# Kernel optimization log

Measured on AMD Instinct MI355X. Metric: run time of the kernel, lower is better.

Reference implementation:

```python
import jax, jax.numpy as jnp
import numpy as np

N = 100000   # nodes
E = 1600000  # edges (avg degree 16)
IN = 128     # in_feats
H = 4        # num_heads
D = 32       # out_feats per head
HD = H * D   # 128
LN_EPS = 1e-5


def setup_inputs() -> dict:
    key = jax.random.key(0)
    ks = jax.random.split(key, 16)
    w = lambda k, shp: (jax.random.normal(k, shp, dtype=jnp.float32) * 0.05)
    feat = jax.random.normal(ks[0], (N, IN), dtype=jnp.float32)
    src = jax.random.randint(ks[1], (E,), 0, N, dtype=jnp.int32)
    # ensure every destination node has >=1 incoming edge (no 0-in-degree)
    dst = jnp.concatenate([
        jnp.arange(N, dtype=jnp.int32),
        jax.random.randint(ks[2], (E - N,), 0, N, dtype=jnp.int32),
    ])
    return {
        "feat": feat, "src": src, "dst": dst,
        "Wq": w(ks[3], (IN, HD)), "bq": jnp.zeros((HD,), jnp.float32),
        "Wk": w(ks[4], (IN, HD)), "bk": jnp.zeros((HD,), jnp.float32),
        "Wv": w(ks[5], (IN, HD)), "bv": jnp.zeros((HD,), jnp.float32),
        "Wskip": w(ks[6], (IN, HD)), "bskip": jnp.zeros((HD,), jnp.float32),
        "Wgate": w(ks[7], (3 * HD, 1)), "bgate": jnp.zeros((1,), jnp.float32),
        "gamma": jnp.ones((HD,), jnp.float32), "beta": jnp.zeros((HD,), jnp.float32),
        "prelu_a": jnp.asarray(0.25, jnp.float32),
    }


def reference(feat, src, dst, Wq, bq, Wk, bk, Wv, bv, Wskip, bskip,
              Wgate, bgate, gamma, beta, prelu_a):
    n = feat.shape[0]
    q = (feat @ Wq + bq).reshape(n, H, D)   # src-side 'ft'
    k = (feat @ Wk + bk).reshape(n, H, D)   # dst-side 'ft'
    v = (feat @ Wv + bv).reshape(n, H, D)
    # edge scores: u_dot_v per head, scaled by 1/sqrt(D)
    a = jnp.einsum('ehd,ehd->eh', q[src], k[dst]) / jnp.sqrt(jnp.float32(D))  # [E,H]
    # edge_softmax: softmax over incoming edges of each destination node
    m = jax.ops.segment_max(a, dst, num_segments=n)          # [N,H]
    ex = jnp.exp(a - m[dst])                                  # [E,H]
    den = jax.ops.segment_sum(ex, dst, num_segments=n)        # [N,H]
    sa = ex / den[dst]                                        # [E,H]
    # weighted scatter-sum aggregation: sum_e sa * v[src] -> dst
    agg = jax.ops.segment_sum(sa[:, :, None] * v[src], dst, num_segments=n)
    rst = agg.reshape(n, HD)
    # skip connection + gate
    skip = feat @ Wskip + bskip
    g = jax.nn.sigmoid(jnp.concatenate([skip, rst, skip - rst], axis=-1) @ Wgate + bgate)
    rst = g * skip + (1.0 - g) * rst
    # layer norm
    mu = jnp.mean(rst, axis=-1, keepdims=True)
    var = jnp.mean(jnp.square(rst - mu), axis=-1, keepdims=True)
    rst = (rst - mu) * jax.lax.rsqrt(var + LN_EPS) * gamma + beta
    # PReLU (single shared slope)
    return jnp.where(rst > 0, rst, prelu_a * rst)
```

## Files before the change

### kernel.cpp

```cpp
#include <hip/hip_runtime.h>
#include <hip/hip_bf16.h>
#include <hip/hip_fp16.h>
#include <math.h>

#define N_NODES 100000
#define N_EDGES 1600000
#define NBUK 196
#define NSB  256
#define EPB  6250

typedef __attribute__((ext_vector_type(8))) short bf16x8;
typedef __attribute__((ext_vector_type(4))) float f32x4;
typedef __attribute__((ext_vector_type(2))) float f32x2;

__device__ __forceinline__ short f2bf_s(float x) {
    __hip_bfloat16 b = __float2bfloat16(x);
    return *reinterpret_cast<short*>(&b);
}
__device__ __forceinline__ __half2 bc2(unsigned u) {
    return *reinterpret_cast<__half2*>(&u);
}
__device__ __forceinline__ unsigned bcu(__half2 h) {
    return *reinterpret_cast<unsigned*>(&h);
}
__device__ __forceinline__ unsigned pack2h(float a, float b) {
    __half ha = __float2half(a), hb = __float2half(b);
    return (unsigned)*reinterpret_cast<unsigned short*>(&ha)
         | ((unsigned)*reinterpret_cast<unsigned short*>(&hb) << 16);
}

__global__ __launch_bounds__(256) void hist2_wt(
    const int* __restrict__ dst,
    const float* __restrict__ Wq, const float* __restrict__ Wk,
    const float* __restrict__ Wv, const float* __restrict__ Ws,
    int* __restrict__ histT, unsigned short* __restrict__ Wtb)
{
    int bid = blockIdx.x, tid = threadIdx.x;
    if (bid < NSB) {
        __shared__ int h[4 * NBUK];
        for (int t = tid; t < 4 * NBUK; t += 256) h[t] = 0;
        __syncthreads();
        int w = tid >> 6;
        for (int i = tid; i < EPB; i += 256)
            atomicAdd(&h[w * NBUK + (dst[bid * EPB + i] >> 9)], 1);
        __syncthreads();
        if (tid < NBUK)
            histT[tid * NSB + bid] = h[tid] + h[NBUK + tid]
                                   + h[2 * NBUK + tid] + h[3 * NBUK + tid];
    } else {
        int j = (bid - NSB) * 256 + tid;
        int m = j >> 14;
        int rem = j & 16383;
        int c = rem >> 7;
        int kk = rem & 127;
        const float* W = (m == 0) ? Wq : (m == 1) ? Wk : (m == 2) ? Wv : Ws;
        Wtb[j] = (unsigned short)f2bf_s(W[(size_t)kk * 128 + c]);
    }
}

__global__ __launch_bounds__(256) void scan_block2(
    const int* __restrict__ in, int* __restrict__ outlocal, int* __restrict__ bsums)
{
    __shared__ int s[256];
    int i = blockIdx.x * 256 + threadIdx.x;
    int x = in[i];
    s[threadIdx.x] = x;
    __syncthreads();
    #pragma unroll
    for (int o = 1; o < 256; o <<= 1) {
        int t = (threadIdx.x >= o) ? s[threadIdx.x - o] : 0;
        __syncthreads();
        s[threadIdx.x] += t;
        __syncthreads();
    }
    outlocal[i] = s[threadIdx.x] - x;
    if (threadIdx.x == 255) bsums[blockIdx.x] = s[255];
}

__global__ __launch_bounds__(512) void scan_sums2(
    const int* __restrict__ bsums, int* __restrict__ bscan)
{
    __shared__ int s[512];
    int i = threadIdx.x;
    int x = (i < NBUK) ? bsums[i] : 0;
    s[i] = x;
    __syncthreads();
    #pragma unroll
    for (int o = 1; o < 512; o <<= 1) {
        int t = (i >= o) ? s[i - o] : 0;
        __syncthreads();
        s[i] += t;
        __syncthreads();
    }
    if (i < NBUK) bscan[i] = s[i] - x;
}

__global__ __launch_bounds__(256) void scatter2(
    const int* __restrict__ src, const int* __restrict__ dst,
    const int* __restrict__ boffs, const int* __restrict__ bscan,
    unsigned* __restrict__ tmp)
{
    __shared__ int cur[NBUK];
    int bid = blockIdx.x, tid = threadIdx.x;
    if (tid < NBUK) cur[tid] = 0;
    __syncthreads();
    for (int i = tid; i < EPB; i += 256) {
        int e = bid * EPB + i;
        int d = dst[e];
        int s = src[e];
        int j = d >> 9;
        int r = atomicAdd(&cur[j], 1);
        int pos = boffs[j * NSB + bid] + bscan[j] + r;
        tmp[pos] = ((unsigned)(d & 511) << 17) | (unsigned)s;
    }
}

__global__ __launch_bounds__(256) void bucket_sort(
    const unsigned* __restrict__ tmp, const int* __restrict__ bscan,
    int* __restrict__ sorted_src, int* __restrict__ offs)
{
    int j = blockIdx.x, tid = threadIdx.x;
    int base = bscan[j];
    int next = (j == NBUK - 1) ? N_EDGES : bscan[j + 1];
    int cnt = next - base;

    __shared__ int h[512];
    __shared__ int o_[512];
    __shared__ int s_[256];

    h[tid] = 0; h[tid + 256] = 0;
    __syncthreads();
    for (int i = tid; i < cnt; i += 256)
        atomicAdd(&h[tmp[base + i] >> 17], 1);
    __syncthreads();

    int a0 = h[2 * tid], a1 = h[2 * tid + 1];
    s_[tid] = a0 + a1;
    __syncthreads();
    #pragma unroll
    for (int o = 1; o < 256; o <<= 1) {
        int t = (tid >= o) ? s_[tid - o] : 0;
        __syncthreads();
        s_[tid] += t;
        __syncthreads();
    }
    int eb = s_[tid] - a0 - a1;
    o_[2 * tid] = eb;
    o_[2 * tid + 1] = eb + a0;
    __syncthreads();

    for (int t = tid; t < 512; t += 256) {
        int n = j * 512 + t;
        if (n < N_NODES) offs[n] = base + o_[t];
    }
    __syncthreads();

    for (int i = tid; i < cnt; i += 256) {
        unsigned rec = tmp[base + i];
        int r = atomicAdd(&o_[rec >> 17], 1);
        sorted_src[base + r] = (int)((rec & 0x1FFFFu) << 7);
    }
}

__global__ __launch_bounds__(256) void gemm_mfma(
    const float* __restrict__ feat, const unsigned short* __restrict__ Wtb,
    const float* __restrict__ bq, const float* __restrict__ bk,
    const float* __restrict__ bv, const float* __restrict__ bs,
    unsigned char* __restrict__ q8, __half* __restrict__ vh,
    __half* __restrict__ ks_)
{
    __shared__ __align__(16) unsigned short Atile[32][136];
    __shared__ __align__(16) unsigned char  Oq8[32][144];
    __shared__ __align__(16) unsigned char  Ovh[32][272];
    __shared__ __align__(16) unsigned char  Oks[32][528];

    const int tid = threadIdx.x;
    const int r0  = blockIdx.x * 32;

    {
        int row = tid >> 3;
        int cg  = (tid & 7) * 16;
        const float4* fp = (const float4*)(feat + (size_t)(r0 + row) * 128 + cg);
        float4 f0 = fp[0], f1 = fp[1], f2 = fp[2], f3 = fp[3];
        unsigned short* ap = &Atile[row][cg];
        ap[0]  = (unsigned short)f2bf_s(f0.x); ap[1]  = (unsigned short)f2bf_s(f0.y);
        ap[2]  = (unsigned short)f2bf_s(f0.z); ap[3]  = (unsigned short)f2bf_s(f0.w);
        ap[4]  = (unsigned short)f2bf_s(f1.x); ap[5]  = (unsigned short)f2bf_s(f1.y);
        ap[6]  = (unsigned short)f2bf_s(f1.z); ap[7]  = (unsigned short)f2bf_s(f1.w);
        ap[8]  = (unsigned short)f2bf_s(f2.x); ap[9]  = (unsigned short)f2bf_s(f2.y);
        ap[10] = (unsigned short)f2bf_s(f2.z); ap[11] = (unsigned short)f2bf_s(f2.w);
        ap[12] = (unsigned short)f2bf_s(f3.x); ap[13] = (unsigned short)f2bf_s(f3.y);
        ap[14] = (unsigned short)f2bf_s(f3.z); ap[15] = (unsigned short)f2bf_s(f3.w);
    }
    __syncthreads();

    const int mat = tid >> 6;
    const int l   = tid & 63;
    const int lr  = l & 15;
    const int lg  = l >> 4;
    const float* bias = (mat == 0) ? bq : (mat == 1) ? bk : (mat == 2) ? bv : bs;

    f32x4 acc[2][8];
    #pragma unroll
    for (int i = 0; i < 2; i++)
        #pragma unroll
        for (int j = 0; j < 8; j++) acc[i][j] = (f32x4){0.f, 0.f, 0.f, 0.f};

    #pragma unroll
    for (int kks = 0; kks < 4; kks++) {
        const int k0 = kks * 32 + lg * 8;
        bf16x8 a[2], b[8];
        #pragma unroll
        for (int rf = 0; rf < 2; rf++)
            a[rf] = *(const bf16x8*)&Atile[rf * 16 + lr][k0];
        #pragma unroll
        for (int cf = 0; cf < 8; cf++) {
            int col = cf * 16 + lr;
            b[cf] = *(const bf16x8*)(Wtb + ((size_t)mat * 128 + col) * 128 + k0);
        }
        #pragma unroll
        for (int rf = 0; rf < 2; rf++)
            #pragma unroll
            for (int cf = 0; cf < 8; cf++)
                acc[rf][cf] = __builtin_amdgcn_mfma_f32_16x16x32_bf16(
                    b[cf], a[rf], acc[rf][cf], 0, 0, 0);
    }

    #pragma unroll
    for (int rf = 0; rf < 2; rf++) {
        int rl = rf * 16 + lr;
        #pragma unroll
        for (int cf = 0; cf < 8; cf++) {
            int colb = cf * 16 + lg * 4;
            float4 b4 = *(const float4*)(bias + colb);
            float a0 = acc[rf][cf][0] + b4.x, a1 = acc[rf][cf][1] + b4.y;
            float a2 = acc[rf][cf][2] + b4.z, a3 = acc[rf][cf][3] + b4.w;
            if (mat == 0) {
                unsigned u = (unsigned)__builtin_amdgcn_cvt_pk_fp8_f32(a0, a1, 0, false);
                u = (unsigned)__builtin_amdgcn_cvt_pk_fp8_f32(a2, a3, (int)u, true);
                *(unsigned*)&Oq8[rl][colb] = u;
            } else if (mat == 2) {
                uint2 pk; pk.x = pack2h(a0, a1); pk.y = pack2h(a2, a3);
                *(uint2*)&Ovh[rl][colb * 2] = pk;
            } else {
                uint2 pk; pk.x = pack2h(a0, a1); pk.y = pack2h(a2, a3);
                *(uint2*)&Oks[rl][((mat == 3) ? 256 : 0) + colb * 2] = pk;
            }
        }
    }
    __syncthreads();

    {
        int row = tid >> 3;
        int c16 = (tid & 7) * 16;
        *(uint4*)(q8 + (size_t)(r0 + row) * 128 + c16) = *(const uint4*)&Oq8[row][c16];
        {
            char* gp = (char*)vh + (size_t)(r0 + row) * 256 + (tid & 7) * 32;
            const char* lp = (const char*)&Ovh[row][0] + (tid & 7) * 32;
            ((uint4*)gp)[0] = ((const uint4*)lp)[0];
            ((uint4*)gp)[1] = ((const uint4*)lp)[1];
        }
        {
            char* gp = (char*)ks_ + (size_t)(r0 + row) * 512 + (tid & 7) * 64;
            const char* lp = (const char*)&Oks[row][0] + (tid & 7) * 64;
            ((uint4*)gp)[0] = ((const uint4*)lp)[0];
            ((uint4*)gp)[1] = ((const uint4*)lp)[1];
            ((uint4*)gp)[2] = ((const uint4*)lp)[2];
            ((uint4*)gp)[3] = ((const uint4*)lp)[3];
        }
    }
}

__global__ __launch_bounds__(256) void node_fused(
    const unsigned char* __restrict__ q8, const __half* __restrict__ vh,
    const __half* __restrict__ ks_,
    const int* __restrict__ offs, const int* __restrict__ sorted_src,
    const float* __restrict__ wg, const float* __restrict__ bg,
    const float* __restrict__ gamma, const float* __restrict__ beta,
    const float* __restrict__ pa, float* __restrict__ out)
{
    int wid = threadIdx.x >> 6;
    int l   = threadIdx.x & 63;
    int qtr = l >> 4;
    int c   = l & 15;
    int n = blockIdx.x * 4 + wid;
    if (n >= N_NODES) return;

    int start = offs[n];
    int end   = (n + 1 < N_NODES) ? offs[n + 1] : N_EDGES;

    const uint4* krow = (const uint4*)ks_;
    uint4 kp  = krow[(size_t)n * 32 + c];
    uint4 sp4 = krow[(size_t)n * 32 + 16 + c];

    float kf[8];
    {
        __half2 h;
        h = bc2(kp.x); kf[0] = __low2float(h); kf[1] = __high2float(h);
        h = bc2(kp.y); kf[2] = __low2float(h); kf[3] = __high2float(h);
        h = bc2(kp.z); kf[4] = __low2float(h); kf[5] = __high2float(h);
        h = bc2(kp.w); kf[6] = __low2float(h); kf[7] = __high2float(h);
    }

    float den = 0.f;
    __half2 ag0 = bc2(0u), ag1 = bc2(0u), ag2 = bc2(0u), ag3 = bc2(0u);
    const float C = 0.25503483f;

    const char* qb = (const char*)q8 + c * 8;
    const char* vb = (const char*)vh + c * 16;

    int base = start;
    int sA = sorted_src[min(base + qtr, end - 1)];
    uint2 qA = *(const uint2*)(qb + sA);
    uint4 vA = *(const uint4*)(vb + 2 * (size_t)sA);
    bool hasB = (base + 4) < end;
    uint2 qB; uint4 vB;
    if (hasB) {
        int sB = sorted_src[min(base + 4 + qtr, end - 1)];
        qB = *(const uint2*)(qb + sB);
        vB = *(const uint4*)(vb + 2 * (size_t)sB);
    }
    int sC = ((base + 8) < end) ? sorted_src[min(base + 8 + qtr, end - 1)] : 0;

    for (;;) {
        bool hasC = (base + 8) < end;
        uint2 qC; uint4 vC;
        if (hasC) {
            qC = *(const uint2*)(qb + sC);
            vC = *(const uint4*)(vb + 2 * (size_t)sC);
        }
        int sD = ((base + 12) < end) ? sorted_src[min(base + 12 + qtr, end - 1)] : 0;

        f32x2 q01 = __builtin_amdgcn_cvt_pk_f32_fp8((int)qA.x, false);
        f32x2 q23 = __builtin_amdgcn_cvt_pk_f32_fp8((int)qA.x, true);
        f32x2 q45 = __builtin_amdgcn_cvt_pk_f32_fp8((int)qA.y, false);
        f32x2 q67 = __builtin_amdgcn_cvt_pk_f32_fp8((int)qA.y, true);
        float d = q01.x * kf[0] + q01.y * kf[1] + q23.x * kf[2] + q23.y * kf[3]
                + q45.x * kf[4] + q45.y * kf[5] + q67.x * kf[6] + q67.y * kf[7];
        d += __shfl_xor(d, 1);
        d += __shfl_xor(d, 2);
        float e = (base + qtr < end) ? __builtin_amdgcn_exp2f(d * C) : 0.f;
        den += e;
        __half2 e2 = __float2half2_rn(e);
        ag0 = __hfma2(e2, bc2(vA.x), ag0);
        ag1 = __hfma2(e2, bc2(vA.y), ag1);
        ag2 = __hfma2(e2, bc2(vA.z), ag2);
        ag3 = __hfma2(e2, bc2(vA.w), ag3);

        if (!hasB) break;
        base += 4;
        qA = qB; vA = vB; qB = qC; vB = vC; sC = sD; hasB = hasC;
    }

    den += __shfl_xor(den, 16);
    den += __shfl_xor(den, 32);
    ag0 = __hadd2(ag0, bc2(__shfl_xor(bcu(ag0), 16)));
    ag1 = __hadd2(ag1, bc2(__shfl_xor(bcu(ag1), 16)));
    ag2 = __hadd2(ag2, bc2(__shfl_xor(bcu(ag2), 16)));
    ag3 = __hadd2(ag3, bc2(__shfl_xor(bcu(ag3), 16)));
    ag0 = __hadd2(ag0, bc2(__shfl_xor(bcu(ag0), 32)));
    ag1 = __hadd2(ag1, bc2(__shfl_xor(bcu(ag1), 32)));
    ag2 = __hadd2(ag2, bc2(__shfl_xor(bcu(ag2), 32)));
    ag3 = __hadd2(ag3, bc2(__shfl_xor(bcu(ag3), 32)));

    float rd = 1.f / den;
    float r[8];
    r[0] = __low2float(ag0) * rd; r[1] = __high2float(ag0) * rd;
    r[2] = __low2float(ag1) * rd; r[3] = __high2float(ag1) * rd;
    r[4] = __low2float(ag2) * rd; r[5] = __high2float(ag2) * rd;
    r[6] = __low2float(ag3) * rd; r[7] = __high2float(ag3) * rd;

    float s[8];
    s[0] = __low2float(bc2(sp4.x)); s[1] = __high2float(bc2(sp4.x));
    s[2] = __low2float(bc2(sp4.y)); s[3] = __high2float(bc2(sp4.y));
    s[4] = __low2float(bc2(sp4.z)); s[5] = __high2float(bc2(sp4.z));
    s[6] = __low2float(bc2(sp4.w)); s[7] = __high2float(bc2(sp4.w));

    const float4* wgf = (const float4*)wg;
    float4 w0a = wgf[2 * c],      w0b = wgf[2 * c + 1];
    float4 w1a = wgf[32 + 2 * c], w1b = wgf[32 + 2 * c + 1];
    float4 w2a = wgf[64 + 2 * c], w2b = wgf[64 + 2 * c + 1];
    float w0[8] = {w0a.x, w0a.y, w0a.z, w0a.w, w0b.x, w0b.y, w0b.z, w0b.w};
    float w1[8] = {w1a.x, w1a.y, w1a.z, w1a.w, w1b.x, w1b.y, w1b.z, w1b.w};
    float w2[8] = {w2a.x, w2a.y, w2a.z, w2a.w, w2b.x, w2b.y, w2b.z, w2b.w};

    float gs = 0.f;
    #pragma unroll
    for (int j = 0; j < 8; j++)
        gs += s[j] * w0[j] + r[j] * w1[j] + (s[j] - r[j]) * w2[j];
    gs += __shfl_xor(gs, 1);
    gs += __shfl_xor(gs, 2);
    gs += __shfl_xor(gs, 4);
    gs += __shfl_xor(gs, 8);
    float g = 1.f / (1.f + __builtin_amdgcn_exp2f(-(gs + bg[0]) * 1.4426950408889634f));

    #pragma unroll
    for (int j = 0; j < 8; j++) r[j] = g * s[j] + (1.f - g) * r[j];

    float mu = 0.f;
    #pragma unroll
    for (int j = 0; j < 8; j++) mu += r[j];
    mu += __shfl_xor(mu, 1);
    mu += __shfl_xor(mu, 2);
    mu += __shfl_xor(mu, 4);
    mu += __shfl_xor(mu, 8);
    mu *= (1.f / 128.f);

    float var = 0.f;
    #pragma unroll
    for (int j = 0; j < 8; j++) { float e0 = r[j] - mu; var += e0 * e0; }
    var += __shfl_xor(var, 1);
    var += __shfl_xor(var, 2);
    var += __shfl_xor(var, 4);
    var += __shfl_xor(var, 8);
    var *= (1.f / 128.f);
    float inv = rsqrtf(var + 1e-5f);

    if (qtr == 0) {
        float4 ga = ((const float4*)gamma)[2 * c], gb = ((const float4*)gamma)[2 * c + 1];
        float4 ba = ((const float4*)beta)[2 * c],  bb = ((const float4*)beta)[2 * c + 1];
        float gm[8] = {ga.x, ga.y, ga.z, ga.w, gb.x, gb.y, gb.z, gb.w};
        float bt[8] = {ba.x, ba.y, ba.z, ba.w, bb.x, bb.y, bb.z, bb.w};
        float al = pa[0];
        float y[8];
        #pragma unroll
        for (int j = 0; j < 8; j++) {
            float t = (r[j] - mu) * inv * gm[j] + bt[j];
            y[j] = (t > 0.f) ? t : al * t;
        }
        float4* op = (float4*)(out + (size_t)n * 128 + c * 8);
        op[0] = (float4){y[0], y[1], y[2], y[3]};
        op[1] = (float4){y[4], y[5], y[6], y[7]};
    }
}

extern "C" void kernel_launch(void* const* d_in, const int* in_sizes, int n_in,
                              void* d_out, int out_size, void* d_ws, size_t ws_size,
                              hipStream_t stream) {
    const float* feat  = (const float*)d_in[0];
    const int*   src   = (const int*)d_in[1];
    const int*   dst   = (const int*)d_in[2];
    const float* Wq    = (const float*)d_in[3];
    const float* bq    = (const float*)d_in[4];
    const float* Wk    = (const float*)d_in[5];
    const float* bk    = (const float*)d_in[6];
    const float* Wv    = (const float*)d_in[7];
    const float* bv    = (const float*)d_in[8];
    const float* Wsk   = (const float*)d_in[9];
    const float* bsk   = (const float*)d_in[10];
    const float* Wg    = (const float*)d_in[11];
    const float* bg    = (const float*)d_in[12];
    const float* gamma = (const float*)d_in[13];
    const float* beta  = (const float*)d_in[14];
    const float* pa    = (const float*)d_in[15];
    float* out = (float*)d_out;

    char* p = (char*)d_ws;
    unsigned char* q8  = (unsigned char*)p;  p += (size_t)N_NODES * 128;
    __half*        vh  = (__half*)p;         p += (size_t)N_NODES * 128 * 2;
    __half*        ks_ = (__half*)p;         p += (size_t)N_NODES * 256 * 2;
    unsigned short* Wtb = (unsigned short*)p;  p += (size_t)4 * 128 * 128 * 2;
    int*      sorted_src = (int*)p;      p += (size_t)N_EDGES * 4;
    unsigned* tmp        = (unsigned*)p; p += (size_t)N_EDGES * 4;
    int*      histT      = (int*)p;      p += (size_t)NBUK * NSB * 4;
    int*      boffs      = (int*)p;      p += (size_t)NBUK * NSB * 4;
    int*      offs       = (int*)p;      p += (size_t)N_NODES * 4;
    int*      bsums      = (int*)p;      p += 4096;
    int*      bscan      = (int*)p;      p += 4096;

    hist2_wt<<<NSB + 256, 256, 0, stream>>>(dst, Wq, Wk, Wv, Wsk, histT, Wtb);
    scan_block2<<<NBUK, 256, 0, stream>>>(histT, boffs, bsums);
    scan_sums2<<<1, 512, 0, stream>>>(bsums, bscan);
    scatter2<<<NSB, 256, 0, stream>>>(src, dst, boffs, bscan, tmp);
    bucket_sort<<<NBUK, 256, 0, stream>>>(tmp, bscan, sorted_src, offs);
    gemm_mfma<<<3125, 256, 0, stream>>>(feat, Wtb, bq, bk, bv, bsk, q8, vh, ks_);
    node_fused<<<(N_NODES + 3) / 4, 256, 0, stream>>>(q8, vh, ks_, offs, sorted_src,
                                                      Wg, bg, gamma, beta, pa, out);
}
```

Baseline: 234.3 us.

## Fuse CSR build kernels into one persistent kernel with grid barriers

New measurement: 321.7 us. 37.3% more time.

```diff
diff --git a/kernel.cpp b/kernel.cpp
--- a/kernel.cpp
+++ b/kernel.cpp
@@ -29,26 +29,36 @@
          | ((unsigned)*reinterpret_cast<unsigned short*>(&hb) << 16);
 }
 
-__global__ __launch_bounds__(256) void hist2_wt(
-    const int* __restrict__ dst,
+__device__ __forceinline__ void gbar(int* cnt, int target) {
+    __syncthreads();
+    if (threadIdx.x == 0) {
+        __hip_atomic_fetch_add(cnt, 1, __ATOMIC_ACQ_REL, __HIP_MEMORY_SCOPE_AGENT);
+        while (__hip_atomic_load(cnt, __ATOMIC_ACQUIRE, __HIP_MEMORY_SCOPE_AGENT) < target)
+            __builtin_amdgcn_s_sleep(2);
+    }
+    __syncthreads();
+}
+
+__global__ __launch_bounds__(256) void csr_build(
+    const int* __restrict__ src, const int* __restrict__ dst,
     const float* __restrict__ Wq, const float* __restrict__ Wk,
     const float* __restrict__ Wv, const float* __restrict__ Ws,
-    int* __restrict__ histT, unsigned short* __restrict__ Wtb)
+    unsigned short* __restrict__ Wtb,
+    int* __restrict__ histT, int* __restrict__ boffs,
+    int* __restrict__ bsums, int* __restrict__ bscan,
+    unsigned* __restrict__ tmp, int* __restrict__ sorted_src,
+    int* __restrict__ offs, int* __restrict__ barcnt)
 {
-    int bid = blockIdx.x, tid = threadIdx.x;
-    if (bid < NSB) {
-        __shared__ int h[4 * NBUK];
-        for (int t = tid; t < 4 * NBUK; t += 256) h[t] = 0;
-        __syncthreads();
+    __shared__ int shm[1280];
+    const int bid = blockIdx.x, tid = threadIdx.x;
+
+    for (int t = tid; t < 4 * NBUK; t += 256) shm[t] = 0;
+    __syncthreads();
+    {
         int w = tid >> 6;
         for (int i = tid; i < EPB; i += 256)
-            atomicAdd(&h[w * NBUK + (dst[bid * EPB + i] >> 9)], 1);
-        __syncthreads();
-        if (tid < NBUK)
-            histT[tid * NSB + bid] = h[tid] + h[NBUK + tid]
-                                   + h[2 * NBUK + tid] + h[3 * NBUK + tid];
-    } else {
-        int j = (bid - NSB) * 256 + tid;
+            atomicAdd(&shm[w * NBUK + (dst[bid * EPB + i] >> 9)], 1);
+        int j = bid * 256 + tid;
         int m = j >> 14;
         int rem = j & 16383;
         int c = rem >> 7;
@@ -56,109 +66,98 @@
         const float* W = (m == 0) ? Wq : (m == 1) ? Wk : (m == 2) ? Wv : Ws;
         Wtb[j] = (unsigned short)f2bf_s(W[(size_t)kk * 128 + c]);
     }
-}
-
-__global__ __launch_bounds__(256) void scan_block2(
-    const int* __restrict__ in, int* __restrict__ outlocal, int* __restrict__ bsums)
-{
-    __shared__ int s[256];
-    int i = blockIdx.x * 256 + threadIdx.x;
-    int x = in[i];
-    s[threadIdx.x] = x;
-    __syncthreads();
-    #pragma unroll
-    for (int o = 1; o < 256; o <<= 1) {
-        int t = (threadIdx.x >= o) ? s[threadIdx.x - o] : 0;
-        __syncthreads();
-        s[threadIdx.x] += t;
-        __syncthreads();
-    }
-    outlocal[i] = s[threadIdx.x] - x;
-    if (threadIdx.x == 255) bsums[blockIdx.x] = s[255];
-}
-
-__global__ __launch_bounds__(512) void scan_sums2(
-    const int* __restrict__ bsums, int* __restrict__ bscan)
-{
-    __shared__ int s[512];
-    int i = threadIdx.x;
-    int x = (i < NBUK) ? bsums[i] : 0;
-    s[i] = x;
-    __syncthreads();
-    #pragma unroll
-    for (int o = 1; o < 512; o <<= 1) {
-        int t = (i >= o) ? s[i - o] : 0;
-        __syncthreads();
-        s[i] += t;
-        __syncthreads();
-    }
-    if (i < NBUK) bscan[i] = s[i] - x;
-}
-
-__global__ __launch_bounds__(256) void scatter2(
-    const int* __restrict__ src, const int* __restrict__ dst,
-    const int* __restrict__ boffs, const int* __restrict__ bscan,
-    unsigned* __restrict__ tmp)
-{
-    __shared__ int cur[NBUK];
-    int bid = blockIdx.x, tid = threadIdx.x;
-    if (tid < NBUK) cur[tid] = 0;
-    __syncthreads();
-    for (int i = tid; i < EPB; i += 256) {
-        int e = bid * EPB + i;
-        int d = dst[e];
-        int s = src[e];
-        int j = d >> 9;
-        int r = atomicAdd(&cur[j], 1);
-        int pos = boffs[j * NSB + bid] + bscan[j] + r;
-        tmp[pos] = ((unsigned)(d & 511) << 17) | (unsigned)s;
-    }
-}
-
-__global__ __launch_bounds__(256) void bucket_sort(
-    const unsigned* __restrict__ tmp, const int* __restrict__ bscan,
-    int* __restrict__ sorted_src, int* __restrict__ offs)
-{
-    int j = blockIdx.x, tid = threadIdx.x;
-    int base = bscan[j];
-    int next = (j == NBUK - 1) ? N_EDGES : bscan[j + 1];
-    int cnt = next - base;
-
-    __shared__ int h[512];
-    __shared__ int o_[512];
-    __shared__ int s_[256];
-
-    h[tid] = 0; h[tid + 256] = 0;
-    __syncthreads();
-    for (int i = tid; i < cnt; i += 256)
-        atomicAdd(&h[tmp[base + i] >> 17], 1);
-    __syncthreads();
-
-    int a0 = h[2 * tid], a1 = h[2 * tid + 1];
-    s_[tid] = a0 + a1;
-    __syncthreads();
-    #pragma unroll
-    for (int o = 1; o < 256; o <<= 1) {
-        int t = (tid >= o) ? s_[tid - o] : 0;
-        __syncthreads();
-        s_[tid] += t;
-        __syncthreads();
-    }
-    int eb = s_[tid] - a0 - a1;
-    o_[2 * tid] = eb;
-    o_[2 * tid + 1] = eb + a0;
-    __syncthreads();
-
-    for (int t = tid; t < 512; t += 256) {
-        int n = j * 512 + t;
-        if (n < N_NODES) offs[n] = base + o_[t];
-    }
-    __syncthreads();
-
-    for (int i = tid; i < cnt; i += 256) {
-        unsigned rec = tmp[base + i];
-        int r = atomicAdd(&o_[rec >> 17], 1);
-        sorted_src[base + r] = (int)((rec & 0x1FFFFu) << 7);
+    __syncthreads();
+    if (tid < NBUK)
+        histT[tid * NSB + bid] = shm[tid] + shm[NBUK + tid]
+                               + shm[2 * NBUK + tid] + shm[3 * NBUK + tid];
+    gbar(barcnt, 1 * NSB);
+
+    if (bid < NBUK) {
+        int x = histT[bid * NSB + tid];
+        shm[tid] = x;
+        __syncthreads();
+        #pragma unroll
+        for (int o = 1; o < 256; o <<= 1) {
+            int t = (tid >= o) ? shm[tid - o] : 0;
+            __syncthreads();
+            shm[tid] += t;
+            __syncthreads();
+        }
+        boffs[bid * NSB + tid] = shm[tid] - x;
+        if (tid == 255) bsums[bid] = shm[255];
+    }
+    gbar(barcnt, 2 * NSB);
+
+    if (bid == 0) {
+        int x = (tid < NBUK) ? bsums[tid] : 0;
+        shm[tid] = x;
+        __syncthreads();
+        #pragma unroll
+        for (int o = 1; o < 256; o <<= 1) {
+            int t = (tid >= o) ? shm[tid - o] : 0;
+            __syncthreads();
+            shm[tid] += t;
+            __syncthreads();
+        }
+        if (tid < NBUK) bscan[tid] = shm[tid] - x;
+    }
+    gbar(barcnt, 3 * NSB);
+
+    {
+        if (tid < NBUK) shm[tid] = 0;
+        __syncthreads();
+        for (int i = tid; i < EPB; i += 256) {
+            int e = bid * EPB + i;
+            int d = dst[e];
+            int s = src[e];
+            int j = d >> 9;
+            int r = atomicAdd(&shm[j], 1);
+            int pos = boffs[j * NSB + bid] + bscan[j] + r;
+            tmp[pos] = ((unsigned)(d & 511) << 17) | (unsigned)s;
+        }
+    }
+    gbar(barcnt, 4 * NSB);
+
+    if (bid < NBUK) {
+        int* h  = shm;
+        int* o_ = shm + 512;
+        int* s_ = shm + 1024;
+        int base = bscan[bid];
+        int next = (bid == NBUK - 1) ? N_EDGES : bscan[bid + 1];
+        int cnt = next - base;
+
+        h[tid] = 0; h[tid + 256] = 0;
+        __syncthreads();
+        for (int i = tid; i < cnt; i += 256)
+            atomicAdd(&h[tmp[base + i] >> 17], 1);
+        __syncthreads();
+
+        int a0 = h[2 * tid], a1 = h[2 * tid + 1];
+        s_[tid] = a0 + a1;
+        __syncthreads();
+        #pragma unroll
+        for (int o = 1; o < 256; o <<= 1) {
+            int t = (tid >= o) ? s_[tid - o] : 0;
+            __syncthreads();
+            s_[tid] += t;
+            __syncthreads();
+        }
+        int eb = s_[tid] - a0 - a1;
+        o_[2 * tid] = eb;
+        o_[2 * tid + 1] = eb + a0;
+        __syncthreads();
+
+        for (int t = tid; t < 512; t += 256) {
+            int n = bid * 512 + t;
+            if (n < N_NODES) offs[n] = base + o_[t];
+        }
+        __syncthreads();
+
+        for (int i = tid; i < cnt; i += 256) {
+            unsigned rec = tmp[base + i];
+            int r = atomicAdd(&o_[rec >> 17], 1);
+            sorted_src[base + r] = (int)((rec & 0x1FFFFu) << 7);
+        }
     }
 }
 
@@ -467,12 +466,12 @@
     int*      offs       = (int*)p;      p += (size_t)N_NODES * 4;
     int*      bsums      = (int*)p;      p += 4096;
     int*      bscan      = (int*)p;      p += 4096;
-
-    hist2_wt<<<NSB + 256, 256, 0, stream>>>(dst, Wq, Wk, Wv, Wsk, histT, Wtb);
-    scan_block2<<<NBUK, 256, 0, stream>>>(histT, boffs, bsums);
-    scan_sums2<<<1, 512, 0, stream>>>(bsums, bscan);
-    scatter2<<<NSB, 256, 0, stream>>>(src, dst, boffs, bscan, tmp);
-    bucket_sort<<<NBUK, 256, 0, stream>>>(tmp, bscan, sorted_src, offs);
+    int*      barcnt     = (int*)p;      p += 4096;
+
+    hipMemsetAsync(barcnt, 0, 4, stream);
+    csr_build<<<NSB, 256, 0, stream>>>(src, dst, Wq, Wk, Wv, Wsk, Wtb,
+                                       histT, boffs, bsums, bscan,
+                                       tmp, sorted_src, offs, barcnt);
     gemm_mfma<<<3125, 256, 0, stream>>>(feat, Wtb, bq, bk, bv, bsk, q8, vh, ks_);
     node_fused<<<(N_NODES + 3) / 4, 256, 0, stream>>>(q8, vh, ks_, offs, sorted_src,
                                                       Wg, bg, gamma, beta, pa, out);
```
